# Performance work log

Hardware: AMD Instinct MI355X
Metric: run time of the kernel (lower is better)

## Reference

```python
import jax, jax.numpy as jnp
import numpy as np

FILTER_SIZE = 5
C_IN = 32
C_OUT = 64
N = 8192


def setup_inputs() -> dict:
    key = jax.random.key(0)
    k1, k2, k3 = jax.random.split(key, 3)
    L = jax.random.normal(k1, (N, N), dtype=jnp.float32) / np.float32(np.sqrt(N))
    x = jax.random.normal(k2, (C_IN, N), dtype=jnp.float32)
    theta = jax.random.normal(k3, (C_OUT, C_IN, FILTER_SIZE), dtype=jnp.float32)  # variance=1.0
    bias = jnp.zeros((C_OUT, 1), dtype=jnp.float32)
    return {"L": L, "x": x, "theta": theta, "bias": bias}


def reference(L, x, theta, bias):
    # Chebyshev recurrence vectorized over all input channels at once.
    # Original does per-channel column matvecs L @ x[c]; here T_k has shape
    # (C_in, N) and L @ x_col per channel == T @ L.T.
    T_prev = x                      # T_0, (C_in, N)
    Ts = [T_prev]
    if FILTER_SIZE > 1:
        T_curr = T_prev @ L.T       # T_1
        Ts.append(T_curr)
        for _ in range(2, FILTER_SIZE):
            T_next = 2.0 * (T_curr @ L.T) - T_prev
            Ts.append(T_next)
            T_prev, T_curr = T_curr, T_next
    X = jnp.stack(Ts, axis=-1)      # (C_in, N, K) — matches torch assemble
    y = jnp.einsum('imk,oik->om', X, theta) + bias  # (C_out, N)
    return y
```

## Files before the change

### kernel.cpp

```cpp
#include <hip/hip_runtime.h>

#define NN 8192
#define CIN 32
#define COUT 64
#define KF 5

typedef __attribute__((ext_vector_type(8))) short bf16x8_t;
typedef __attribute__((ext_vector_type(4))) float f32x4_t;

typedef const __attribute__((address_space(1))) void* as1_t;
typedef __attribute__((address_space(3))) void* as3_t;
__device__ __forceinline__ void gll16(const void* g, void* l) {
    __builtin_amdgcn_global_load_lds((as1_t)g, (as3_t)l, 16, 0, 0);
}

__device__ __forceinline__ short f2bf(float f) {
    unsigned u = __builtin_bit_cast(unsigned, f);
    unsigned r = (u + 0x7FFFu + ((u >> 16) & 1u)) >> 16;
    return (short)(unsigned short)r;
}

__device__ __forceinline__ bf16x8_t cvt8(float4 a, float4 b) {
    bf16x8_t v;
    v[0] = f2bf(a.x); v[1] = f2bf(a.y); v[2] = f2bf(a.z); v[3] = f2bf(a.w);
    v[4] = f2bf(b.x); v[5] = f2bf(b.y); v[6] = f2bf(b.z); v[7] = f2bf(b.w);
    return v;
}

__global__ void cvt_kernel(const float* __restrict__ src, short* __restrict__ dst) {
    int idx = blockIdx.x * 256 + threadIdx.x;
    float4 v = reinterpret_cast<const float4*>(src)[idx];
    short4 o;
    o.x = f2bf(v.x); o.y = f2bf(v.y); o.z = f2bf(v.z); o.w = f2bf(v.w);
    reinterpret_cast<short4*>(dst)[idx] = o;
}

__device__ __forceinline__ void stash_partials(float* red, int wave, int g, int r,
                                               const f32x4_t& acc0, const f32x4_t& acc1) {
    const int base = wave * 512 + g * 64 + r;
#pragma unroll
    for (int t = 0; t < 4; ++t) {
        red[base + t * 16]       = acc0[t];
        red[base + t * 16 + 256] = acc1[t];
    }
}

__device__ __forceinline__ float reduce8(const float* red, int tid) {
    float s = red[tid];
#pragma unroll
    for (int w = 1; w < 8; ++w) s += red[w * 512 + tid];
    return s;
}

__device__ __forceinline__ void mid_core(const char* __restrict__ LbW,
                                         const short* __restrict__ Abase,
                                         int wave, int lane, char* stg,
                                         f32x4_t& acc0, f32x4_t& acc1)
{
    const int g = lane >> 4, r = lane & 15;
    const int kw = wave * 1024;
    const char* srcL = LbW + lane * 16;
    const short* sA0 = Abase + (size_t)(lane & 31) * NN + kw + (lane >> 5) * 8;

#pragma unroll
    for (int c0 = 0; c0 < 2; ++c0) {
        char* Ld = stg + c0 * 6144;
        char* Ad = Ld + 2048;
        gll16(srcL + c0 * 2048,        Ld);
        gll16(srcL + c0 * 2048 + 1024, Ld + 1024);
#pragma unroll
        for (int j = 0; j < 4; ++j) gll16(sA0 + c0 * 64 + j * 16, Ad + j * 1024);
    }

    for (int c = 0; c < 16; ++c) {
        if (c < 15) asm volatile("s_waitcnt vmcnt(6)" ::: "memory");
        else        asm volatile("s_waitcnt vmcnt(0)" ::: "memory");
        const char* Ld = stg + (c & 1) * 6144;
        const char* Ad = Ld + 2048;
#pragma unroll
        for (int kk = 0; kk < 2; ++kk) {
            bf16x8_t b  = *(const bf16x8_t*)(Ld + (kk * 4 + g) * 256 + r * 16);
            bf16x8_t a0 = *(const bf16x8_t*)(Ad + (kk * 4 + g) * 512 + r * 16);
            bf16x8_t a1 = *(const bf16x8_t*)(Ad + (kk * 4 + g) * 512 + 256 + r * 16);
            acc0 = __builtin_amdgcn_mfma_f32_16x16x32_bf16(a0, b, acc0, 0, 0, 0);
            acc1 = __builtin_amdgcn_mfma_f32_16x16x32_bf16(a1, b, acc1, 0, 0, 0);
        }
        if (c < 14) {
            asm volatile("s_waitcnt lgkmcnt(0)" ::: "memory");
            const int cn = c + 2;
            char* Ldn = stg + (cn & 1) * 6144;
            char* Adn = Ldn + 2048;
            gll16(srcL + cn * 2048,        Ldn);
            gll16(srcL + cn * 2048 + 1024, Ldn + 1024);
#pragma unroll
            for (int j = 0; j < 4; ++j) gll16(sA0 + cn * 64 + j * 16, Adn + j * 1024);
        }
    }
}

__global__ __launch_bounds__(512, 2) void pass1_kernel(
    const float* __restrict__ L, const short* __restrict__ Tb0,
    char* __restrict__ LbC, float* __restrict__ Tf1, short* __restrict__ Tb1)
{
    __shared__ float red[4096];
    __shared__ __align__(16) char stg[8][16384];
    const int tid = threadIdx.x, wave = tid >> 6, lane = tid & 63;
    const int g = lane >> 4, r = lane & 15;
    const int t = blockIdx.x, i0 = t * 16;
    const int kw = wave * 1024;
    char* st = stg[wave];

    const int ls = lane >> 4, cb = (lane & 15) * 16;
    const float* baseL[4];
#pragma unroll
    for (int j = 0; j < 4; ++j) {
        const int row = 4 * j + ls;
        baseL[j] = L + (size_t)(i0 + row) * NN + kw + ((cb ^ ((row & 7) << 4)) >> 2);
    }
    const short* sA0 = Tb0 + (size_t)(lane & 31) * NN + kw + (lane >> 5) * 8;
    char* LbW = LbC + (size_t)t * 262144 + wave * 32768;

#pragma unroll
    for (int c0 = 0; c0 < 2; ++c0) {
        char* Ld = st + c0 * 8192;
        char* Ad = Ld + 4096;
#pragma unroll
        for (int j = 0; j < 4; ++j) gll16(baseL[j] + c0 * 64, Ld + j * 1024);
#pragma unroll
        for (int j = 0; j < 4; ++j) gll16(sA0 + c0 * 64 + j * 16, Ad + j * 1024);
    }

    f32x4_t acc0 = {0.f,0.f,0.f,0.f}, acc1 = {0.f,0.f,0.f,0.f};
    const int Xr = (r & 7) << 4;
    for (int c = 0; c < 16; ++c) {
        if (c == 0)      asm volatile("s_waitcnt vmcnt(8)" ::: "memory");
        else if (c < 15) asm volatile("s_waitcnt vmcnt(10)" ::: "memory");
        else             asm volatile("s_waitcnt vmcnt(2)" ::: "memory");
        const char* Ld = st + (c & 1) * 8192;
        const char* Ad = Ld + 4096;
#pragma unroll
        for (int kk = 0; kk < 2; ++kk) {
            float4 l0 = *(const float4*)(Ld + r * 256 + ((kk * 128 + g * 32) ^ Xr));
            float4 l1 = *(const float4*)(Ld + r * 256 + ((kk * 128 + g * 32 + 16) ^ Xr));
            bf16x8_t b = cvt8(l0, l1);
            *(bf16x8_t*)(LbW + c * 2048 + kk * 1024 + lane * 16) = b;
            bf16x8_t a0 = *(const bf16x8_t*)(Ad + (kk * 4 + g) * 512 + r * 16);
            bf16x8_t a1 = *(const bf16x8_t*)(Ad + (kk * 4 + g) * 512 + 256 + r * 16);
            acc0 = __builtin_amdgcn_mfma_f32_16x16x32_bf16(a0, b, acc0, 0, 0, 0);
            acc1 = __builtin_amdgcn_mfma_f32_16x16x32_bf16(a1, b, acc1, 0, 0, 0);
        }
        if (c < 14) {
            asm volatile("s_waitcnt lgkmcnt(0)" ::: "memory");
            const int cn = c + 2;
            char* Ldn = st + (cn & 1) * 8192;
            char* Adn = Ldn + 4096;
#pragma unroll
            for (int j = 0; j < 4; ++j) gll16(baseL[j] + cn * 64, Ldn + j * 1024);
#pragma unroll
            for (int j = 0; j < 4; ++j) gll16(sA0 + cn * 64 + j * 16, Adn + j * 1024);
        }
    }

    stash_partials(red, wave, g, r, acc0, acc1);
    __syncthreads();
    const int c = tid >> 4, il = tid & 15;
    const float val = reduce8(red, tid);
    const size_t off = (size_t)c * NN + i0 + il;
    Tf1[off] = val;
    Tb1[off] = f2bf(val);
}

__global__ __launch_bounds__(512, 2) void passmid_kernel(
    const char* __restrict__ LbC, const short* __restrict__ A,
    const float* __restrict__ Tprev, float* __restrict__ Tf, short* __restrict__ Tb)
{
    __shared__ float red[4096];
    __shared__ __align__(16) char stg[8][12288];
    const int tid = threadIdx.x, wave = tid >> 6, lane = tid & 63;
    const int g = lane >> 4, r = lane & 15;
    const int t = blockIdx.x, i0 = t * 16;

    f32x4_t acc0 = {0.f,0.f,0.f,0.f}, acc1 = {0.f,0.f,0.f,0.f};
    mid_core(LbC + (size_t)t * 262144 + wave * 32768, A, wave, lane, stg[wave], acc0, acc1);

    stash_partials(red, wave, g, r, acc0, acc1);
    __syncthreads();
    const int c = tid >> 4, il = tid & 15;
    const size_t off = (size_t)c * NN + i0 + il;
    const float val = 2.0f * reduce8(red, tid) - Tprev[off];
    Tf[off] = val;
    Tb[off] = f2bf(val);
}

__global__ __launch_bounds__(512, 2) void pass4_kernel(
    const char* __restrict__ LbC, const short* __restrict__ A,
    const float* __restrict__ Tf2, const float* __restrict__ x,
    const float* __restrict__ Tf1, const float* __restrict__ Tf3,
    const float* __restrict__ theta, const float* __restrict__ bias,
    float* __restrict__ y)
{
    __shared__ float red[4096];
    __shared__ __align__(16) char stg[8][12288];
    const int tid = threadIdx.x, wave = tid >> 6, lane = tid & 63;
    const int g = lane >> 4, r = lane & 15;
    const int t = blockIdx.x, i0 = t * 16;

    f32x4_t acc0 = {0.f,0.f,0.f,0.f}, acc1 = {0.f,0.f,0.f,0.f};
    mid_core(LbC + (size_t)t * 262144 + wave * 32768, A, wave, lane, stg[wave], acc0, acc1);

    stash_partials(red, wave, g, r, acc0, acc1);
    __syncthreads();
    {
        const int c = tid >> 4, il = tid & 15;
        red[tid] = 2.0f * reduce8(red, tid) - Tf2[(size_t)c * NN + i0 + il];
    }
    __syncthreads();

    const int o = tid >> 4, il = tid & 15;
    float a0 = bias[o], a1 = bias[o + 32];
    for (int cc = 0; cc < CIN; ++cc) {
        const size_t off = (size_t)cc * NN + i0 + il;
        const float t0 = x[off], t1 = Tf1[off], t2 = Tf2[off], t3 = Tf3[off];
        const float t4 = red[cc * 16 + il];
        const float* th0 = theta + ((size_t)o * CIN + cc) * KF;
        const float* th1 = theta + ((size_t)(o + 32) * CIN + cc) * KF;
        a0 += t0 * th0[0] + t1 * th0[1] + t2 * th0[2] + t3 * th0[3] + t4 * th0[4];
        a1 += t0 * th1[0] + t1 * th1[1] + t2 * th1[2] + t3 * th1[3] + t4 * th1[4];
    }
    y[(size_t)o * NN + i0 + il]        = a0;
    y[(size_t)(o + 32) * NN + i0 + il] = a1;
}

extern "C" void kernel_launch(void* const* d_in, const int* in_sizes, int n_in,
                              void* d_out, int out_size, void* d_ws, size_t ws_size,
                              hipStream_t stream) {
    const float* L     = (const float*)d_in[0];
    const float* x     = (const float*)d_in[1];
    const float* theta = (const float*)d_in[2];
    const float* bias  = (const float*)d_in[3];
    float* y = (float*)d_out;

    const size_t TE = (size_t)CIN * NN;
    const size_t LE = (size_t)NN * NN;

    char*  LbC = (char*)d_ws;
    float* Tf1 = (float*)(LbC + LE * 2);
    float* Tf2 = Tf1 + TE;
    float* Tf3 = Tf2 + TE;
    short* Tb0 = (short*)(Tf3 + TE);
    short* Tb1 = Tb0 + TE;
    short* Tb2 = Tb1 + TE;
    short* Tb3 = Tb2 + TE;

    cvt_kernel<<<256, 256, 0, stream>>>(x, Tb0);
    pass1_kernel<<<NN / 16, 512, 0, stream>>>(L, Tb0, LbC, Tf1, Tb1);
    passmid_kernel<<<NN / 16, 512, 0, stream>>>(LbC, Tb1, x,   Tf2, Tb2);
    passmid_kernel<<<NN / 16, 512, 0, stream>>>(LbC, Tb2, Tf1, Tf3, Tb3);
    pass4_kernel<<<NN / 16, 512, 0, stream>>>(LbC, Tb3, Tf2, x, Tf1, Tf3,
                                              theta, bias, y);
}
```

Baseline: 252.1 us.

## Replace LDS-staged pipelined pass1 with direct global loads into MFMA

```diff
diff --git a/kernel.cpp b/kernel.cpp
--- a/kernel.cpp
+++ b/kernel.cpp
@@ -50,6 +50,43 @@
 #pragma unroll
     for (int w = 1; w < 8; ++w) s += red[w * 512 + tid];
     return s;
+}
+
+__global__ __launch_bounds__(512, 4) void pass1_kernel(
+    const float* __restrict__ L, const short* __restrict__ Tb0,
+    char* __restrict__ LbC, float* __restrict__ Tf1, short* __restrict__ Tb1)
+{
+    __shared__ float red[4096];
+    const int tid = threadIdx.x, wave = tid >> 6, lane = tid & 63;
+    const int g = lane >> 4, r = lane & 15;
+    const int t = blockIdx.x, i0 = t * 16;
+    const int kw = wave * 1024;
+
+    const float* Lrow = L   + (size_t)(i0 + r) * NN + kw + g * 8;
+    const short* A0   = Tb0 + (size_t)r * NN        + kw + g * 8;
+    const short* A1   = Tb0 + (size_t)(r + 16) * NN + kw + g * 8;
+    char* LbW = LbC + (size_t)t * 262144 + wave * 32768 + lane * 16;
+
+    f32x4_t acc0 = {0.f,0.f,0.f,0.f}, acc1 = {0.f,0.f,0.f,0.f};
+    for (int it = 0; it < 32; ++it) {
+        const int jl = it * 32;
+        float4 l0 = *(const float4*)(Lrow + jl);
+        float4 l1 = *(const float4*)(Lrow + jl + 4);
+        bf16x8_t a0 = *(const bf16x8_t*)(A0 + jl);
+        bf16x8_t a1 = *(const bf16x8_t*)(A1 + jl);
+        bf16x8_t b = cvt8(l0, l1);
+        *(bf16x8_t*)(LbW + it * 1024) = b;
+        acc0 = __builtin_amdgcn_mfma_f32_16x16x32_bf16(a0, b, acc0, 0, 0, 0);
+        acc1 = __builtin_amdgcn_mfma_f32_16x16x32_bf16(a1, b, acc1, 0, 0, 0);
+    }
+
+    stash_partials(red, wave, g, r, acc0, acc1);
+    __syncthreads();
+    const int c = tid >> 4, il = tid & 15;
+    const float val = reduce8(red, tid);
+    const size_t off = (size_t)c * NN + i0 + il;
+    Tf1[off] = val;
+    Tb1[off] = f2bf(val);
 }
 
 __device__ __forceinline__ void mid_core(const char* __restrict__ LbW,
@@ -98,78 +135,6 @@
     }
 }
 
-__global__ __launch_bounds__(512, 2) void pass1_kernel(
-    const float* __restrict__ L, const short* __restrict__ Tb0,
-    char* __restrict__ LbC, float* __restrict__ Tf1, short* __restrict__ Tb1)
-{
-    __shared__ float red[4096];
-    __shared__ __align__(16) char stg[8][16384];
-    const int tid = threadIdx.x, wave = tid >> 6, lane = tid & 63;
-    const int g = lane >> 4, r = lane & 15;
-    const int t = blockIdx.x, i0 = t * 16;
-    const int kw = wave * 1024;
-    char* st = stg[wave];
-
-    const int ls = lane >> 4, cb = (lane & 15) * 16;
-    const float* baseL[4];
-#pragma unroll
-    for (int j = 0; j < 4; ++j) {
-        const int row = 4 * j + ls;
-        baseL[j] = L + (size_t)(i0 + row) * NN + kw + ((cb ^ ((row & 7) << 4)) >> 2);
-    }
-    const short* sA0 = Tb0 + (size_t)(lane & 31) * NN + kw + (lane >> 5) * 8;
-    char* LbW = LbC + (size_t)t * 262144 + wave * 32768;
-
-#pragma unroll
-    for (int c0 = 0; c0 < 2; ++c0) {
-        char* Ld = st + c0 * 8192;
-        char* Ad = Ld + 4096;
-#pragma unroll
-        for (int j = 0; j < 4; ++j) gll16(baseL[j] + c0 * 64, Ld + j * 1024);
-#pragma unroll
-        for (int j = 0; j < 4; ++j) gll16(sA0 + c0 * 64 + j * 16, Ad + j * 1024);
-    }
-
-    f32x4_t acc0 = {0.f,0.f,0.f,0.f}, acc1 = {0.f,0.f,0.f,0.f};
-    const int Xr = (r & 7) << 4;
-    for (int c = 0; c < 16; ++c) {
-        if (c == 0)      asm volatile("s_waitcnt vmcnt(8)" ::: "memory");
-        else if (c < 15) asm volatile("s_waitcnt vmcnt(10)" ::: "memory");
-        else             asm volatile("s_waitcnt vmcnt(2)" ::: "memory");
-        const char* Ld = st + (c & 1) * 8192;
-        const char* Ad = Ld + 4096;
-#pragma unroll
-        for (int kk = 0; kk < 2; ++kk) {
-            float4 l0 = *(const float4*)(Ld + r * 256 + ((kk * 128 + g * 32) ^ Xr));
-            float4 l1 = *(const float4*)(Ld + r * 256 + ((kk * 128 + g * 32 + 16) ^ Xr));
-            bf16x8_t b = cvt8(l0, l1);
-            *(bf16x8_t*)(LbW + c * 2048 + kk * 1024 + lane * 16) = b;
-            bf16x8_t a0 = *(const bf16x8_t*)(Ad + (kk * 4 + g) * 512 + r * 16);
-            bf16x8_t a1 = *(const bf16x8_t*)(Ad + (kk * 4 + g) * 512 + 256 + r * 16);
-            acc0 = __builtin_amdgcn_mfma_f32_16x16x32_bf16(a0, b, acc0, 0, 0, 0);
-            acc1 = __builtin_amdgcn_mfma_f32_16x16x32_bf16(a1, b, acc1, 0, 0, 0);
-        }
-        if (c < 14) {
-            asm volatile("s_waitcnt lgkmcnt(0)" ::: "memory");
-            const int cn = c + 2;
-            char* Ldn = st + (cn & 1) * 8192;
-            char* Adn = Ldn + 4096;
-#pragma unroll
-            for (int j = 0; j < 4; ++j) gll16(baseL[j] + cn * 64, Ldn + j * 1024);
-#pragma unroll
-            for (int j = 0; j < 4; ++j) gll16(sA0 + cn * 64 + j * 16, Adn + j * 1024);
-        }
-    }
-
-    stash_partials(red, wave, g, r, acc0, acc1);
-    __syncthreads();
-    const int c = tid >> 4, il = tid & 15;
-    const float val = reduce8(red, tid);
-    const size_t off = (size_t)c * NN + i0 + il;
-    Tf1[off] = val;
-    Tb1[off] = f2bf(val);
-}
-
 __global__ __launch_bounds__(512, 2) void passmid_kernel(
     const char* __restrict__ LbC, const short* __restrict__ A,
     const float* __restrict__ Tprev, float* __restrict__ Tf, short* __restrict__ Tb)
```

After: 248.6 us. Within noise of the previous version (-1.4%).
